# Optimization experiments

Hardware: AMD Instinct MI355X
Metric: run time of the kernel (lower is better)

## Reference

```python
import jax, jax.numpy as jnp
import numpy as np

B, L, E, H, NBF = 4, 4096, 512, 8, 256
D = E // H          # head_dim = 64
CHUNK = 256         # chunk size for exact causal linear attention
EPS = 1e-4          # stabilizer from performer softmax_kernel


def _orth_proj(nb, d, seed=0):
    """Gaussian orthogonal random features matrix [nb, d] (FAVOR+, scaling=0)."""
    rng = np.random.default_rng(seed)
    blocks = []
    n_full = nb // d
    for _ in range(n_full):
        q, _ = np.linalg.qr(rng.standard_normal((d, d)))
        blocks.append(q.T)
    rem = nb - n_full * d
    if rem:
        q, _ = np.linalg.qr(rng.standard_normal((d, d)))
        blocks.append(q.T[:rem])
    proj = np.concatenate(blocks, 0)
    mult = np.linalg.norm(rng.standard_normal((nb, d)), axis=1)  # chi(d) row scales
    return (mult[:, None] * proj).astype(np.float32)


def setup_inputs() -> dict:
    key = jax.random.key(0)
    ks = jax.random.split(key, 7)
    g = lambda k, sh: jax.random.normal(k, sh, dtype=jnp.float32)
    return {
        "queries": g(ks[0], (B, L, E)),
        "keys": g(ks[1], (B, L, E)),
        "values": g(ks[2], (B, L, E)),
        "Wq": g(ks[3], (D, D)) / np.float32(np.sqrt(D)),
        "Wk": g(ks[4], (D, D)) / np.float32(np.sqrt(D)),
        "Wv": g(ks[5], (D, D)) / np.float32(np.sqrt(D)),
        "Wout": g(ks[6], (E, E)) / np.float32(np.sqrt(E)),
        "bout": jnp.zeros((E,), jnp.float32),
        "proj": jnp.asarray(_orth_proj(NBF, D)),
    }


def _softmax_kernel(x, proj, is_query):
    # x: [B,H,L,D], proj: [M,D]  -> phi(x): [B,H,L,M]
    dn = x.shape[-1] ** -0.25
    ratio = proj.shape[0] ** -0.5
    xd = jnp.einsum('bhld,md->bhlm', x * dn, proj)
    diag = 0.5 * (dn ** 2) * jnp.sum(x * x, axis=-1, keepdims=True)
    if is_query:
        m = jnp.max(xd, axis=-1, keepdims=True)
    else:
        m = jnp.max(xd)
    return ratio * (jnp.exp(xd - diag - m) + EPS)


def _causal_linear_attn(qp, kp, v, chunk=CHUNK):
    # Exact causal linear attention via chunked prefix-state scan (no [B,H,L,M,D] tensor).
    Bn, Hn, Ln, M = qp.shape
    Dv = v.shape[-1]
    n = Ln // chunk
    qc = qp.reshape(Bn, Hn, n, chunk, M).transpose(2, 0, 1, 3, 4)
    kc = kp.reshape(Bn, Hn, n, chunk, M).transpose(2, 0, 1, 3, 4)
    vc = v.reshape(Bn, Hn, n, chunk, Dv).transpose(2, 0, 1, 3, 4)
    mask = jnp.tril(jnp.ones((chunk, chunk), qp.dtype))

    def step(carry, xs):
        S, z = carry                      # S:[B,H,M,D], z:[B,H,M]
        q, k, vv = xs                     # [B,H,C,M], [B,H,C,M], [B,H,C,D]
        scores = jnp.einsum('bhim,bhjm->bhij', q, k) * mask
        num = jnp.einsum('bhim,bhmd->bhid', q, S) + jnp.einsum('bhij,bhjd->bhid', scores, vv)
        den = jnp.einsum('bhim,bhm->bhi', q, z) + scores.sum(-1)
        out = num / den[..., None]
        S = S + jnp.einsum('bhjm,bhjd->bhmd', k, vv)
        z = z + k.sum(axis=2)
        return (S, z), out

    S0 = jnp.zeros((Bn, Hn, M, Dv), qp.dtype)
    z0 = jnp.zeros((Bn, Hn, M), qp.dtype)
    _, out = jax.lax.scan(step, (S0, z0), (qc, kc, vc))
    return out.transpose(1, 2, 0, 3, 4).reshape(Bn, Hn, Ln, Dv)


def reference(queries, keys, values, Wq, Wk, Wv, Wout, bout, proj):
    split = lambda x: x.reshape(B, L, H, D).transpose(0, 2, 1, 3)  # [B,H,L,D]
    q = split(queries) @ Wq.T
    k = split(keys) @ Wk.T
    v = split(values) @ Wv.T
    qp = _softmax_kernel(q, proj, True)
    kp = _softmax_kernel(k, proj, False)
    attn = _causal_linear_attn(qp, kp, v)
    attn = attn.transpose(0, 2, 1, 3).reshape(B, L, E)
    return attn @ Wout.T + bout
```

## Files before the change

### kernel.cpp

```cpp
#include <hip/hip_runtime.h>
#include <hip/hip_bf16.h>


#define BB 4
#define LL 4096
#define EE 512
#define HH 8
#define DD 64
#define MM 256
#define CC 128
#define NCH 32
#define BHN 32

constexpr float DN    = 0.35355339059327373f;
constexpr float DIAGC = 0.0625f;
constexpr float RATIO = 0.0625f;
constexpr float EPSV  = 1e-4f;
constexpr float L2E   = 1.4426950408889634f;
constexpr float CEPS  = 6.25e-6f;

typedef __attribute__((ext_vector_type(8))) short bf16x8;
typedef __attribute__((ext_vector_type(4))) float f32x4;
union FU { uint4 u; bf16x8 b; };
__device__ __forceinline__ bf16x8 asb(uint4 u){ FU f; f.u = u; return f.b; }
union PK8 { unsigned short s[8]; uint4 u; };
union PK4 { unsigned short s[4]; uint2 u; };

__device__ __forceinline__ unsigned short f2bf(float f){
  unsigned u = __float_as_uint(f);
  u = u + 0x7FFFu + ((u >> 16) & 1u);
  return (unsigned short)(u >> 16);
}
__device__ __forceinline__ float bfl(unsigned u){ return __uint_as_float(u << 16); }
__device__ __forceinline__ unsigned bfpair(float lo, float hi){
  return (unsigned)f2bf(lo) | ((unsigned)f2bf(hi) << 16);
}
__device__ __forceinline__ float pexp(float x, float nb){
  return exp2f(fmaf(x, L2E, nb)) + CEPS;
}
__device__ __forceinline__ unsigned enc_f32(float f){
  unsigned u = __float_as_uint(f);
  return (u & 0x80000000u) ? ~u : (u | 0x80000000u);
}
__device__ __forceinline__ float dec_f32(unsigned u){
  unsigned v = (u & 0x80000000u) ? (u & 0x7FFFFFFFu) : ~u;
  return __uint_as_float(v);
}
__device__ __forceinline__ uint4 pack8(float4 a, float4 b){
  PK8 p;
  p.s[0] = f2bf(a.x); p.s[1] = f2bf(a.y); p.s[2] = f2bf(a.z); p.s[3] = f2bf(a.w);
  p.s[4] = f2bf(b.x); p.s[5] = f2bf(b.y); p.s[6] = f2bf(b.z); p.s[7] = f2bf(b.w);
  return p.u;
}

__global__ __launch_bounds__(256) void k_cvt(const float* __restrict__ Wout,
                                             unsigned short* __restrict__ Woutb,
                                             const float* __restrict__ proj,
                                             unsigned short* __restrict__ projb){
  int bid = blockIdx.x, tid = threadIdx.x;
  if (bid < 512){
    int idx = bid * 256 + tid;
    float2 v = reinterpret_cast<const float2*>(Wout)[idx];
    reinterpret_cast<unsigned*>(Woutb)[idx] = bfpair(v.x, v.y);
  } else {
    int idx = (bid - 512) * 256 + tid;
    float2 v = reinterpret_cast<const float2*>(proj)[idx];
    reinterpret_cast<unsigned*>(projb)[idx] = bfpair(v.x * DN, v.y * DN);
  }
}

__global__ __launch_bounds__(256) void k_qkv(const float* __restrict__ xq,
                                             const float* __restrict__ xk,
                                             const float* __restrict__ xv,
                                             const float* __restrict__ Wq,
                                             const float* __restrict__ Wk,
                                             const float* __restrict__ Wv,
                                             unsigned short* __restrict__ qhb,
                                             unsigned short* __restrict__ khb,
                                             unsigned short* __restrict__ vTb,
                                             float* __restrict__ rsq,
                                             float* __restrict__ rsk){
  __shared__ unsigned short Wl[3 * 64 * 64];
  int tid = threadIdx.x;
  for (int idx = tid; idx < 3 * 64 * 8; idx += 256){
    int sel = idx >> 9, rem = idx & 511, row = rem >> 3, ch = rem & 7;
    const float* Wp = sel == 0 ? Wq : (sel == 1 ? Wk : Wv);
    const float4* w4 = reinterpret_cast<const float4*>(Wp) + row * 16 + ch * 2;
    int byte = sel * 8192 + row * 128 + ((ch * 16) ^ ((row & 7) << 4));
    *reinterpret_cast<uint4*>(reinterpret_cast<char*>(Wl) + byte) = pack8(w4[0], w4[1]);
  }
  __syncthreads();
  int w = tid >> 6, lane = tid & 63, l15 = lane & 15, g = lane >> 4;
  int bh = blockIdx.x >> 5, lb = blockIdx.x & 31;
  int b = bh >> 3, h = bh & 7;
  const char* Wc = reinterpret_cast<const char*>(Wl);
  #pragma unroll
  for (int tt = 0; tt < 2; ++tt){
    int lt = w * 2 + tt;
    int l = lb * 128 + lt * 16 + l15;
    size_t xoff = ((size_t)(b * LL + l)) * EE + h * DD;
    const float4* q4 = reinterpret_cast<const float4*>(xq + xoff);
    const float4* k4 = reinterpret_cast<const float4*>(xk + xoff);
    const float4* v4 = reinterpret_cast<const float4*>(xv + xoff);
    uint4 fq[2], fk[2], fv[2];
    #pragma unroll
    for (int ks = 0; ks < 2; ++ks){
      int fi = ks * 8 + g * 2;
      fq[ks] = pack8(q4[fi], q4[fi + 1]);
      fk[ks] = pack8(k4[fi], k4[fi + 1]);
      fv[ks] = pack8(v4[fi], v4[fi + 1]);
    }
    size_t grow = (size_t)bh * LL + l;
    {
      float ss = 0.f;
      #pragma unroll
      for (int dt = 0; dt < 4; ++dt){
        int row = dt * 16 + l15;
        f32x4 acc = {0.f, 0.f, 0.f, 0.f};
        #pragma unroll
        for (int ks = 0; ks < 2; ++ks){
          int byte = 0 * 8192 + row * 128 + ((ks * 64 + g * 16) ^ ((row & 7) << 4));
          uint4 wf = *reinterpret_cast<const uint4*>(Wc + byte);
          acc = __builtin_amdgcn_mfma_f32_16x16x32_bf16(asb(wf), asb(fq[ks]), acc, 0, 0, 0);
        }
        ss += acc[0]*acc[0] + acc[1]*acc[1] + acc[2]*acc[2] + acc[3]*acc[3];
        ushort4 pk;
        pk.x = f2bf(acc[0]); pk.y = f2bf(acc[1]); pk.z = f2bf(acc[2]); pk.w = f2bf(acc[3]);
        *reinterpret_cast<ushort4*>(qhb + grow * 64 + dt * 16 + g * 4) = pk;
      }
      ss += __shfl_xor(ss, 16, 64);
      ss += __shfl_xor(ss, 32, 64);
      if (g == 0) rsq[grow] = ss;
    }
    {
      float ss = 0.f;
      #pragma unroll
      for (int dt = 0; dt < 4; ++dt){
        int row = dt * 16 + l15;
        f32x4 acc = {0.f, 0.f, 0.f, 0.f};
        #pragma unroll
        for (int ks = 0; ks < 2; ++ks){
          int byte = 1 * 8192 + row * 128 + ((ks * 64 + g * 16) ^ ((row & 7) << 4));
          uint4 wf = *reinterpret_cast<const uint4*>(Wc + byte);
          acc = __builtin_amdgcn_mfma_f32_16x16x32_bf16(asb(wf), asb(fk[ks]), acc, 0, 0, 0);
        }
        ss += acc[0]*acc[0] + acc[1]*acc[1] + acc[2]*acc[2] + acc[3]*acc[3];
        ushort4 pk;
        pk.x = f2bf(acc[0]); pk.y = f2bf(acc[1]); pk.z = f2bf(acc[2]); pk.w = f2bf(acc[3]);
        *reinterpret_cast<ushort4*>(khb + grow * 64 + dt * 16 + g * 4) = pk;
      }
      ss += __shfl_xor(ss, 16, 64);
      ss += __shfl_xor(ss, 32, 64);
      if (g == 0) rsk[grow] = ss;
    }
    #pragma unroll
    for (int dt = 0; dt < 4; ++dt){
      int row = dt * 16 + l15;
      f32x4 acc = {0.f, 0.f, 0.f, 0.f};
      #pragma unroll
      for (int ks = 0; ks < 2; ++ks){
        int byte = 2 * 8192 + row * 128 + ((ks * 64 + g * 16) ^ ((row & 7) << 4));
        uint4 wf = *reinterpret_cast<const uint4*>(Wc + byte);
        acc = __builtin_amdgcn_mfma_f32_16x16x32_bf16(asb(fv[ks]), asb(wf), acc, 0, 0, 0);
      }
      ushort4 pk;
      pk.x = f2bf(acc[0]); pk.y = f2bf(acc[1]); pk.z = f2bf(acc[2]); pk.w = f2bf(acc[3]);
      *reinterpret_cast<ushort4*>(vTb + ((size_t)(bh * DD + dt * 16 + l15)) * LL
                                  + lb * 128 + lt * 16 + g * 4) = pk;
    }
  }
}

__global__ __launch_bounds__(256) void k_kmaxM(const unsigned short* __restrict__ khb,
                                               const unsigned short* __restrict__ projb,
                                               unsigned* __restrict__ kmaxp){
  __shared__ float red[4];
  int tid = threadIdx.x;
  int w = tid >> 6, lane = tid & 63, l15 = lane & 15, g = lane >> 4;
  const uint4* kh4 = reinterpret_cast<const uint4*>(khb);
  const uint4* pj4 = reinterpret_cast<const uint4*>(projb);
  uint4 pa0[16], pa1[16];
  #pragma unroll
  for (int mt = 0; mt < 16; ++mt){
    pa0[mt] = pj4[(size_t)(mt * 16 + l15) * 8 + g];
    pa1[mt] = pj4[(size_t)(mt * 16 + l15) * 8 + 4 + g];
  }
  float mx = -3.0e38f;
  #pragma unroll
  for (int it = 0; it < 8; ++it){
    int rb = blockIdx.x * 4 + w + it * 1024;
    size_t row = (size_t)rb * 16 + l15;
    uint4 kb0 = kh4[row * 8 + g];
    uint4 kb1 = kh4[row * 8 + 4 + g];
    #pragma unroll
    for (int mt = 0; mt < 16; ++mt){
      f32x4 acc = {0.f, 0.f, 0.f, 0.f};
      acc = __builtin_amdgcn_mfma_f32_16x16x32_bf16(asb(pa0[mt]), asb(kb0), acc, 0, 0, 0);
      acc = __builtin_amdgcn_mfma_f32_16x16x32_bf16(asb(pa1[mt]), asb(kb1), acc, 0, 0, 0);
      mx = fmaxf(mx, fmaxf(fmaxf(acc[0], acc[1]), fmaxf(acc[2], acc[3])));
    }
  }
  #pragma unroll
  for (int off = 32; off >= 1; off >>= 1)
    mx = fmaxf(mx, __shfl_xor(mx, off, 64));
  if (lane == 0) red[w] = mx;
  __syncthreads();
  if (tid == 0){
    float m = fmaxf(fmaxf(red[0], red[1]), fmaxf(red[2], red[3]));
    atomicMax(kmaxp, enc_f32(m));
  }
}

__global__ __launch_bounds__(256, 2) void k_chunkKV6(const unsigned short* __restrict__ khb,
                                                     const unsigned short* __restrict__ projb,
                                                     const float* __restrict__ rsk,
                                                     const unsigned* __restrict__ kmaxp,
                                                     const unsigned short* __restrict__ vTb,
                                                     unsigned short* __restrict__ SpT,
                                                     float* __restrict__ zf){
  __shared__ unsigned kL[4 * 128 * 33];
  int tid = threadIdx.x;
  int w = tid >> 6, lane = tid & 63, l15 = lane & 15, g = lane >> 4;
  int blk = blockIdx.x;
  int bh = blk >> 5, c = blk & 31;
  float km = dec_f32(*kmaxp);
  const uint4* kh4 = reinterpret_cast<const uint4*>(khb);
  const uint4* pj4 = reinterpret_cast<const uint4*>(projb);
  const uint4* vTu = reinterpret_cast<const uint4*>(vTb);
  unsigned* kLw = kL + w * 128 * 33;
  const unsigned short* kL16w = reinterpret_cast<const unsigned short*>(kLw);

  uint4 kf0[8], kf1[8];
  float nbk[8];
  #pragma unroll
  for (int jt = 0; jt < 8; ++jt){
    size_t jrow = (size_t)bh * LL + c * CC + jt * 16 + l15;
    kf0[jt] = kh4[jrow * 8 + g];
    kf1[jt] = kh4[jrow * 8 + 4 + g];
    nbk[jt] = -fmaf(fmaf(DIAGC, rsk[jrow], km), L2E, 4.0f);
  }
  #pragma unroll
  for (int mt = 0; mt < 4; ++mt){
    int mrow = w * 64 + mt * 16 + l15;
    uint4 a0 = pj4[(size_t)mrow * 8 + g];
    uint4 a1 = pj4[(size_t)mrow * 8 + 4 + g];
    #pragma unroll
    for (int jt = 0; jt < 8; ++jt){
      f32x4 acc = {0.f, 0.f, 0.f, 0.f};
      acc = __builtin_amdgcn_mfma_f32_16x16x32_bf16(asb(a0), asb(kf0[jt]), acc, 0, 0, 0);
      acc = __builtin_amdgcn_mfma_f32_16x16x32_bf16(asb(a1), asb(kf1[jt]), acc, 0, 0, 0);
      int dwi = (jt * 16 + l15) * 33 + mt * 8 + g * 2;
      kLw[dwi]     = bfpair(pexp(acc[0], nbk[jt]), pexp(acc[1], nbk[jt]));
      kLw[dwi + 1] = bfpair(pexp(acc[2], nbk[jt]), pexp(acc[3], nbk[jt]));
    }
  }

  uint4 vf[4][4];
  #pragma unroll
  for (int dt = 0; dt < 4; ++dt)
    #pragma unroll
    for (int ks = 0; ks < 4; ++ks)
      vf[dt][ks] = vTu[((size_t)(bh * DD + dt * 16 + l15)) * 512 + c * 16 + ks * 4 + g];

  uint4 zero4 = {0u, 0u, 0u, 0u};
  uint4 ones4 = {0x3F803F80u, 0x3F803F80u, 0x3F803F80u, 0x3F803F80u};
  uint4 onesf = (l15 == 0) ? ones4 : zero4;

  #pragma unroll
  for (int mtr = 0; mtr < 4; ++mtr){
    f32x4 acc[4];
    #pragma unroll
    for (int dt = 0; dt < 4; ++dt) acc[dt] = (f32x4){0.f, 0.f, 0.f, 0.f};
    f32x4 accz = {0.f, 0.f, 0.f, 0.f};
    #pragma unroll
    for (int ks = 0; ks < 4; ++ks){
      PK8 p;
      #pragma unroll
      for (int e = 0; e < 8; ++e)
        p.s[e] = kL16w[(ks * 32 + g * 8 + e) * 66 + mtr * 16 + l15];
      bf16x8 kfb = asb(p.u);
      #pragma unroll
      for (int dt = 0; dt < 4; ++dt)
        acc[dt] = __builtin_amdgcn_mfma_f32_16x16x32_bf16(kfb, asb(vf[dt][ks]), acc[dt], 0, 0, 0);
      accz = __builtin_amdgcn_mfma_f32_16x16x32_bf16(kfb, asb(onesf), accz, 0, 0, 0);
    }
    int m0 = w * 64 + mtr * 16;
    #pragma unroll
    for (int dt = 0; dt < 4; ++dt){
      ushort4 pk;
      pk.x = f2bf(acc[dt][0]); pk.y = f2bf(acc[dt][1]);
      pk.z = f2bf(acc[dt][2]); pk.w = f2bf(acc[dt][3]);
      *reinterpret_cast<ushort4*>(SpT + ((size_t)blk * DD + dt * 16 + l15) * MM + m0 + g * 4) = pk;
    }
    if (l15 == 0){
      float4 o; o.x = accz[0]; o.y = accz[1]; o.z = accz[2]; o.w = accz[3];
      *reinterpret_cast<float4*>(zf + (size_t)blk * MM + m0 + g * 4) = o;
    }
  }
}

__global__ __launch_bounds__(256) void k_prefix(unsigned short* __restrict__ buf,
                                                const float* __restrict__ zf,
                                                unsigned short* __restrict__ zb){
  int bid = blockIdx.x, tid = threadIdx.x;
  if (bid < 512){
    const int per4 = (DD * MM) / 4;
    int idx = bid * 256 + tid;
    int bh = idx / per4, r4 = idx - bh * per4;
    float run[4];
    #pragma unroll
    for (int e = 0; e < 4; ++e) run[e] = 0.f;
    for (int c = 0; c < NCH; ++c){
      size_t a = (((size_t)bh * NCH + c) * (DD * MM)) >> 2;
      uint2* p = reinterpret_cast<uint2*>(buf) + a + r4;
      uint2 v = *p;
      PK4 t; t.u = v;
      PK4 o;
      #pragma unroll
      for (int e = 0; e < 4; ++e){
        o.s[e] = f2bf(run[e]);
        run[e] += bfl((unsigned)t.s[e]);
      }
      *p = o.u;
    }
  } else {
    const int per8 = MM / 8;
    int idx = (bid - 512) * 256 + tid;
    int bh = idx / per8, r8 = idx - bh * per8;
    float run[8];
    #pragma unroll
    for (int e = 0; e < 8; ++e) run[e] = 0.f;
    for (int c = 0; c < NCH; ++c){
      size_t base = ((size_t)bh * NCH + c) * MM + r8 * 8;
      float4 v0 = *reinterpret_cast<const float4*>(zf + base);
      float4 v1 = *reinterpret_cast<const float4*>(zf + base + 4);
      PK8 o;
      #pragma unroll
      for (int e = 0; e < 8; ++e) o.s[e] = f2bf(run[e]);
      run[0] += v0.x; run[1] += v0.y; run[2] += v0.z; run[3] += v0.w;
      run[4] += v1.x; run[5] += v1.y; run[6] += v1.z; run[7] += v1.w;
      *reinterpret_cast<uint4*>(zb + base) = o.u;
    }
  }
}

__global__ __launch_bounds__(256, 2) void k_cattn12(const unsigned short* __restrict__ qhb,
                                                    const unsigned short* __restrict__ khb,
                                                    const unsigned short* __restrict__ projb,
                                                    const float* __restrict__ rsq,
                                                    const float* __restrict__ rsk,
                                                    const unsigned* __restrict__ kmaxp,
                                                    const unsigned short* __restrict__ vTb,
                                                    const unsigned short* __restrict__ Spb,
                                                    const unsigned short* __restrict__ zb,
                                                    unsigned short* __restrict__ attnb){
  __shared__ unsigned LDSU[20480];
  char* lds = reinterpret_cast<char*>(LDSU);
  int tid = threadIdx.x;
  int w = tid >> 6, lane = tid & 63, l15 = lane & 15, g = lane >> 4;
  int blk = blockIdx.x;
  int bh = blk >> 5, c = blk & 31;
  int b = bh >> 3, h = bh & 7;
  size_t grow0 = (size_t)bh * LL + c * CC;
  float km = dec_f32(*kmaxp);
  const uint4* qh4 = reinterpret_cast<const uint4*>(qhb);
  const uint4* kh4 = reinterpret_cast<const uint4*>(khb);
  const uint4* pj4 = reinterpret_cast<const uint4*>(projb);
  const uint4* vTu = reinterpret_cast<const uint4*>(vTb);
  const uint4* Spu = reinterpret_cast<const uint4*>(Spb);
  const uint4* zbu = reinterpret_cast<const uint4*>(zb);
  uint4 zero4 = {0u, 0u, 0u, 0u};
  uint4 ones4 = {0x3F803F80u, 0x3F803F80u, 0x3F803F80u, 0x3F803F80u};
  int swz = (l15 & 7) << 4;

  {
    uint4 kf0[8], kf1[8];
    float nbk[8];
    #pragma unroll
    for (int jt = 0; jt < 8; ++jt){
      size_t jrow = grow0 + jt * 16 + l15;
      kf0[jt] = kh4[jrow * 8 + g];
      kf1[jt] = kh4[jrow * 8 + 4 + g];
      nbk[jt] = -fmaf(fmaf(DIAGC, rsk[jrow], km), L2E, 4.0f);
    }
    #pragma unroll
    for (int mt = 0; mt < 4; ++mt){
      int mrow = w * 64 + mt * 16 + l15;
      uint4 a0 = pj4[(size_t)mrow * 8 + g];
      uint4 a1 = pj4[(size_t)mrow * 8 + 4 + g];
      #pragma unroll
      for (int jt = 0; jt < 8; ++jt){
        int jr = jt * 16 + l15;
        f32x4 acc = {0.f, 0.f, 0.f, 0.f};
        acc = __builtin_amdgcn_mfma_f32_16x16x32_bf16(asb(a0), asb(kf0[jt]), acc, 0, 0, 0);
        acc = __builtin_amdgcn_mfma_f32_16x16x32_bf16(asb(a1), asb(kf1[jt]), acc, 0, 0, 0);
        uint2 u;
        u.x = bfpair(pexp(acc[0], nbk[jt]), pexp(acc[1], nbk[jt]));
        u.y = bfpair(pexp(acc[2], nbk[jt]), pexp(acc[3], nbk[jt]));
        int byte = jr * 512 + ((w * 128 + mt * 32 + g * 8) ^ ((jr & 7) << 4));
        *reinterpret_cast<uint2*>(lds + byte) = u;
      }
    }
  }

  int its[2] = { w, 7 - w };
  int swb = 65536 + w * 4096 + l15 * 256;
  uint4 qf[2][8];
  f32x4 acc[2][5];
  {
    size_t irow0 = grow0 + its[0] * 16 + l15;
    size_t irow1 = grow0 + its[1] * 16 + l15;
    uint4 qb0_0 = qh4[irow0 * 8 + g];
    uint4 qb1_0 = qh4[irow0 * 8 + 4 + g];
    uint4 qb0_1 = qh4[irow1 * 8 + g];
    uint4 qb1_1 = qh4[irow1 * 8 + 4 + g];
    f32x4 aq0[16], aq1[16];
    #pragma unroll
    for (int mt = 0; mt < 16; ++mt){
      uint4 a0 = pj4[(size_t)(mt * 16 + l15) * 8 + g];
      uint4 a1 = pj4[(size_t)(mt * 16 + l15) * 8 + 4 + g];
      f32x4 x0 = {0.f, 0.f, 0.f, 0.f};
      x0 = __builtin_amdgcn_mfma_f32_16x16x32_bf16(asb(a0), asb(qb0_0), x0, 0, 0, 0);
      aq0[mt] = __builtin_amdgcn_mfma_f32_16x16x32_bf16(asb(a1), asb(qb1_0), x0, 0, 0, 0);
      f32x4 x1 = {0.f, 0.f, 0.f, 0.f};
      x1 = __builtin_amdgcn_mfma_f32_16x16x32_bf16(asb(a0), asb(qb0_1), x1, 0, 0, 0);
      aq1[mt] = __builtin_amdgcn_mfma_f32_16x16x32_bf16(asb(a1), asb(qb1_1), x1, 0, 0, 0);
    }
    {
      float mx = -3.0e38f;
      #pragma unroll
      for (int mt = 0; mt < 16; ++mt)
        mx = fmaxf(mx, fmaxf(fmaxf(aq0[mt][0], aq0[mt][1]), fmaxf(aq0[mt][2], aq0[mt][3])));
      mx = fmaxf(mx, __shfl_xor(mx, 16, 64));
      mx = fmaxf(mx, __shfl_xor(mx, 32, 64));
      float nb = -fmaf(fmaf(DIAGC, rsq[irow0], mx), L2E, 4.0f);
      #pragma unroll
      for (int half = 0; half < 2; ++half){
        #pragma unroll
        for (int mt = 0; mt < 8; ++mt){
          f32x4 a = aq0[half * 8 + mt];
          uint2 u;
          u.x = bfpair(pexp(a[0], nb), pexp(a[1], nb));
          u.y = bfpair(pexp(a[2], nb), pexp(a[3], nb));
          int byte = swb + ((mt * 32 + g * 8) ^ swz);
          *reinterpret_cast<uint2*>(lds + byte) = u;
        }
        #pragma unroll
        for (int ks = 0; ks < 4; ++ks){
          int byte = swb + ((ks * 64 + g * 16) ^ swz);
          qf[0][half * 4 + ks] = *reinterpret_cast<const uint4*>(lds + byte);
        }
      }
    }
    {
      float mx = -3.0e38f;
      #pragma unroll
      for (int mt = 0; mt < 16; ++mt)
        mx = fmaxf(mx, fmaxf(fmaxf(aq1[mt][0], aq1[mt][1]), fmaxf(aq1[mt][2], aq1[mt][3])));
      mx = fmaxf(mx, __shfl_xor(mx, 16, 64));
      mx = fmaxf(mx, __shfl_xor(mx, 32, 64));
      float nb = -fmaf(fmaf(DIAGC, rsq[irow1], mx), L2E, 4.0f);
      #pragma unroll
      for (int half = 0; half < 2; ++half){
        #pragma unroll
        for (int mt = 0; mt < 8; ++mt){
          f32x4 a = aq1[half * 8 + mt];
          uint2 u;
          u.x = bfpair(pexp(a[0], nb), pexp(a[1], nb));
          u.y = bfpair(pexp(a[2], nb), pexp(a[3], nb));
          int byte = swb + ((mt * 32 + g * 8) ^ swz);
          *reinterpret_cast<uint2*>(lds + byte) = u;
        }
        #pragma unroll
        for (int ks = 0; ks < 4; ++ks){
          int byte = swb + ((ks * 64 + g * 16) ^ swz);
          qf[1][half * 4 + ks] = *reinterpret_cast<const uint4*>(lds + byte);
        }
      }
    }
  }

  #pragma unroll
  for (int t = 0; t < 2; ++t)
    #pragma unroll
    for (int a5 = 0; a5 < 5; ++a5) acc[t][a5] = (f32x4){0.f, 0.f, 0.f, 0.f};
  #pragma unroll
  for (int ks = 0; ks < 8; ++ks){
    bf16x8 q0 = asb(qf[0][ks]);
    bf16x8 q1 = asb(qf[1][ks]);
    #pragma unroll
    for (int dt = 0; dt < 4; ++dt){
      uint4 spf = Spu[((size_t)blk * DD + dt * 16 + l15) * 32 + ks * 4 + g];
      acc[0][dt] = __builtin_amdgcn_mfma_f32_16x16x32_bf16(asb(spf), q0, acc[0][dt], 0, 0, 0);
      acc[1][dt] = __builtin_amdgcn_mfma_f32_16x16x32_bf16(asb(spf), q1, acc[1][dt], 0, 0, 0);
    }
    uint4 zfr = (l15 == 0) ? zbu[blk * 32 + ks * 4 + g] : zero4;
    acc[0][4] = __builtin_amdgcn_mfma_f32_16x16x32_bf16(asb(zfr), q0, acc[0][4], 0, 0, 0);
    acc[1][4] = __builtin_amdgcn_mfma_f32_16x16x32_bf16(asb(zfr), q1, acc[1][4], 0, 0, 0);
  }

  uint4 vf[4][4];
  #pragma unroll
  for (int dt = 0; dt < 4; ++dt)
    #pragma unroll
    for (int ks = 0; ks < 4; ++ks)
      vf[dt][ks] = vTu[((size_t)(bh * DD + dt * 16 + l15)) * 512 + c * 16 + ks * 4 + g];
  __syncthreads();

  #pragma unroll
  for (int t = 0; t < 2; ++t){
    int it = its[t];
    int i = it * 16 + l15;
    int jtmax = it | 1;
    #pragma unroll
    for (int jt = 0; jt < 8; ++jt){
      if (jt <= jtmax){
        f32x4 sa0 = {0.f, 0.f, 0.f, 0.f};
        f32x4 sa1 = {0.f, 0.f, 0.f, 0.f};
        int jr = jt * 16 + l15;
        __builtin_amdgcn_s_setprio(1);
        #pragma unroll
        for (int ks = 0; ks < 4; ++ks){
          int byte0 = jr * 512 + (((2 * ks) * 64 + g * 16) ^ ((jr & 7) << 4));
          int byte1 = jr * 512 + (((2 * ks + 1) * 64 + g * 16) ^ ((jr & 7) << 4));
          uint4 kfu0 = *reinterpret_cast<const uint4*>(lds + byte0);
          uint4 kfu1 = *reinterpret_cast<const uint4*>(lds + byte1);
          sa0 = __builtin_amdgcn_mfma_f32_16x16x32_bf16(asb(kfu0), asb(qf[t][2 * ks]), sa0, 0, 0, 0);
          sa1 = __builtin_amdgcn_mfma_f32_16x16x32_bf16(asb(kfu1), asb(qf[t][2 * ks + 1]), sa1, 0, 0, 0);
        }
        __builtin_amdgcn_s_setprio(0);
        f32x4 sa = sa0 + sa1;
        int jb = jt * 16 + g * 4;
        uint2 u;
        u.x = bfpair((jb + 0 <= i) ? sa[0] : 0.f, (jb + 1 <= i) ? sa[1] : 0.f);
        u.y = bfpair((jb + 2 <= i) ? sa[2] : 0.f, (jb + 3 <= i) ? sa[3] : 0.f);
        int byte = swb + ((jt * 32 + g * 8) ^ swz);
        *reinterpret_cast<uint2*>(lds + byte) = u;
      }
    }
    int ksmax = it >> 1;
    #pragma unroll
    for (int ks = 0; ks < 4; ++ks){
      if (ks <= ksmax){
        int byte = swb + ((ks * 64 + g * 16) ^ swz);
        uint4 sfu = *reinterpret_cast<const uint4*>(lds + byte);
        bf16x8 sf = asb(sfu);
        __builtin_amdgcn_s_setprio(1);
        #pragma unroll
        for (int dt = 0; dt < 4; ++dt)
          acc[t][dt] = __builtin_amdgcn_mfma_f32_16x16x32_bf16(asb(vf[dt][ks]), sf, acc[t][dt], 0, 0, 0);
        uint4 of = (l15 == 0) ? ones4 : zero4;
        acc[t][4] = __builtin_amdgcn_mfma_f32_16x16x32_bf16(asb(of), sf, acc[t][4], 0, 0, 0);
        __builtin_amdgcn_s_setprio(0);
      }
    }
    float den = __shfl(acc[t][4][0], l15, 64);
    float inv = 1.f / den;
    size_t obase = ((size_t)(b * LL + c * CC + i)) * EE + h * DD;
    #pragma unroll
    for (int dt = 0; dt < 4; ++dt){
      ushort4 pk;
      pk.x = f2bf(acc[t][dt][0] * inv); pk.y = f2bf(acc[t][dt][1] * inv);
      pk.z = f2bf(acc[t][dt][2] * inv); pk.w = f2bf(acc[t][dt][3] * inv);
      *reinterpret_cast<ushort4*>(attnb + obase + dt * 16 + g * 4) = pk;
    }
  }
}

__global__ __launch_bounds__(256, 2) void k_proj_M2(const unsigned short* __restrict__ attnb,
                                                    const unsigned short* __restrict__ Woutb,
                                                    const float* __restrict__ bout,
                                                    float* __restrict__ out){
  __shared__ unsigned short Wl[64 * 512];
  int tid = threadIdx.x;
  int w = tid >> 6, lane = tid & 63, l15 = lane & 15, g = lane >> 4;
  int rb = blockIdx.x & 63, eb = blockIdx.x >> 6;
  int r0 = rb * 256, e0 = eb * 64;
  const uint4* at4 = reinterpret_cast<const uint4*>(attnb);
  const uint4* Wo4 = reinterpret_cast<const uint4*>(Woutb);
  for (int idx = tid; idx < 4096; idx += 256){
    int row = idx >> 6, rest = idx & 63, kt = rest >> 3, ch = rest & 7;
    uint4 v = Wo4[(size_t)(e0 + row) * 64 + kt * 8 + ch];
    int byte = kt * 8192 + row * 128 + ((ch * 16) ^ ((row & 7) << 4));
    *reinterpret_cast<uint4*>(reinterpret_cast<char*>(Wl) + byte) = v;
  }
  __syncthreads();
  const char* Wc = reinterpret_cast<const char*>(Wl);
  f32x4 acc[4][4];
  #pragma unroll
  for (int rt = 0; rt < 4; ++rt)
    #pragma unroll
    for (int ct = 0; ct < 4; ++ct) acc[rt][ct] = (f32x4){0.f, 0.f, 0.f, 0.f};
  size_t rbase = (size_t)(r0 + w * 64 + l15) * 64;
  #pragma unroll 4
  for (int ks = 0; ks < 16; ++ks){
    uint4 bfr[4];
    #pragma unroll
    for (int rt = 0; rt < 4; ++rt)
      bfr[rt] = at4[rbase + (size_t)rt * 16 * 64 + ks * 4 + g];
    int kt = ks >> 1, k2 = ks & 1;
    #pragma unroll
    for (int ct = 0; ct < 4; ++ct){
      int row = ct * 16 + l15;
      int byte = kt * 8192 + row * 128 + ((k2 * 64 + g * 16) ^ ((row & 7) << 4));
      uint4 af = *reinterpret_cast<const uint4*>(Wc + byte);
      bf16x8 afb = asb(af);
      #pragma unroll
      for (int rt = 0; rt < 4; ++rt)
        acc[rt][ct] = __builtin_amdgcn_mfma_f32_16x16x32_bf16(afb, asb(bfr[rt]), acc[rt][ct], 0, 0, 0);
    }
  }
  #pragma unroll
  for (int ct = 0; ct < 4; ++ct){
    int e = e0 + ct * 16 + g * 4;
    float4 bo = *reinterpret_cast<const float4*>(bout + e);
    #pragma unroll
    for (int rt = 0; rt < 4; ++rt){
      int r = r0 + w * 64 + rt * 16 + l15;
      float4 o;
      o.x = acc[rt][ct][0] + bo.x; o.y = acc[rt][ct][1] + bo.y;
      o.z = acc[rt][ct][2] + bo.z; o.w = acc[rt][ct][3] + bo.w;
      *reinterpret_cast<float4*>(out + (size_t)r * EE + e) = o;
    }
  }
}

extern "C" void kernel_launch(void* const* d_in, const int* in_sizes, int n_in,
                              void* d_out, int out_size, void* d_ws, size_t ws_size,
                              hipStream_t stream){
  const float* queries = (const float*)d_in[0];
  const float* keys    = (const float*)d_in[1];
  const float* values  = (const float*)d_in[2];
  const float* Wq      = (const float*)d_in[3];
  const float* Wk      = (const float*)d_in[4];
  const float* Wv      = (const float*)d_in[5];
  const float* Wout    = (const float*)d_in[6];
  const float* bout    = (const float*)d_in[7];
  const float* proj    = (const float*)d_in[8];

  char* ws = (char*)d_ws;
  unsigned short* qhb  = (unsigned short*)(ws + 0);
  unsigned short* khb  = (unsigned short*)(ws + 16777216);
  unsigned short* vTb  = (unsigned short*)(ws + 33554432);
  unsigned short* SpT  = (unsigned short*)(ws + 50331648);
  unsigned short* attnb= (unsigned short*)(ws + 83886080);
  float*          zfbuf= (float*)(ws + 100663296);
  unsigned short* zb   = (unsigned short*)(ws + 101711872);
  float*          rsq  = (float*)(ws + 102236160);
  float*          rsk  = (float*)(ws + 102760448);
  unsigned short* Woutb= (unsigned short*)(ws + 103284736);
  unsigned short* projb= (unsigned short*)(ws + 103809024);
  unsigned*       kmax = (unsigned*)(ws + 103841792);
  float*          out  = (float*)d_out;

  hipMemsetAsync(kmax, 0, 4, stream);

  k_cvt<<<dim3(544), dim3(256), 0, stream>>>(Wout, Woutb, proj, projb);

  k_qkv<<<dim3(BHN * 32), dim3(256), 0, stream>>>(queries, keys, values, Wq, Wk, Wv,
                                                  qhb, khb, vTb, rsq, rsk);

  k_kmaxM<<<dim3(256), dim3(256), 0, stream>>>(khb, projb, kmax);

  k_chunkKV6<<<dim3(BHN * NCH), dim3(256), 0, stream>>>(khb, projb, rsk, kmax, vTb, SpT, zfbuf);

  k_prefix<<<dim3(516), dim3(256), 0, stream>>>(SpT, zfbuf, zb);

  k_cattn12<<<dim3(BHN * NCH), dim3(256), 0, stream>>>(qhb, khb, projb, rsq, rsk, kmax,
                                                       vTb, SpT, zb, attnb);

  k_proj_M2<<<dim3(512), dim3(256), 0, stream>>>(attnb, Woutb, bout, out);
}
```

Measured before the change: 190.7 us.

## Fold key max reduction into QKV kernel using premultiplied proj·Wk matrix

Precomputes a bf16 matrix equal to proj times Wk, scaled by DN, in the conversion kernel. The QKV kernel then computes key feature logits straight from the raw key fragments and reduces the global max with an atomic. This removes the separate k_kmaxM launch and its re-read of khb. The max is now taken from logits built with a differently rounded product, so it may differ slightly from the logits used later. The prefix-scan loops also get unroll pragmas.

Measured after the change: 205.8 us. 7.9% more time.

```diff
diff --git a/kernel.cpp b/kernel.cpp
--- a/kernel.cpp
+++ b/kernel.cpp
@@ -56,16 +56,26 @@
 __global__ __launch_bounds__(256) void k_cvt(const float* __restrict__ Wout,
                                              unsigned short* __restrict__ Woutb,
                                              const float* __restrict__ proj,
-                                             unsigned short* __restrict__ projb){
+                                             unsigned short* __restrict__ projb,
+                                             const float* __restrict__ Wk,
+                                             unsigned short* __restrict__ PWb){
   int bid = blockIdx.x, tid = threadIdx.x;
   if (bid < 512){
     int idx = bid * 256 + tid;
     float2 v = reinterpret_cast<const float2*>(Wout)[idx];
     reinterpret_cast<unsigned*>(Woutb)[idx] = bfpair(v.x, v.y);
-  } else {
+  } else if (bid < 544){
     int idx = (bid - 512) * 256 + tid;
     float2 v = reinterpret_cast<const float2*>(proj)[idx];
     reinterpret_cast<unsigned*>(projb)[idx] = bfpair(v.x * DN, v.y * DN);
+  } else {
+    int idx = (bid - 544) * 256 + tid;
+    int m = idx >> 6, dp = idx & 63;
+    float s = 0.f;
+    #pragma unroll 8
+    for (int d = 0; d < 64; ++d)
+      s += proj[m * 64 + d] * Wk[d * 64 + dp];
+    PWb[idx] = f2bf(DN * s);
   }
 }
 
@@ -75,12 +85,15 @@
                                              const float* __restrict__ Wq,
                                              const float* __restrict__ Wk,
                                              const float* __restrict__ Wv,
+                                             const unsigned short* __restrict__ PWb,
                                              unsigned short* __restrict__ qhb,
                                              unsigned short* __restrict__ khb,
                                              unsigned short* __restrict__ vTb,
                                              float* __restrict__ rsq,
-                                             float* __restrict__ rsk){
+                                             float* __restrict__ rsk,
+                                             unsigned* __restrict__ kmaxp){
   __shared__ unsigned short Wl[3 * 64 * 64];
+  __shared__ float red[4];
   int tid = threadIdx.x;
   for (int idx = tid; idx < 3 * 64 * 8; idx += 256){
     int sel = idx >> 9, rem = idx & 511, row = rem >> 3, ch = rem & 7;
@@ -94,6 +107,8 @@
   int bh = blockIdx.x >> 5, lb = blockIdx.x & 31;
   int b = bh >> 3, h = bh & 7;
   const char* Wc = reinterpret_cast<const char*>(Wl);
+  const uint4* pw4 = reinterpret_cast<const uint4*>(PWb);
+  float mxk = -3.0e38f;
   #pragma unroll
   for (int tt = 0; tt < 2; ++tt){
     int lt = w * 2 + tt;
@@ -154,6 +169,15 @@
       if (g == 0) rsk[grow] = ss;
     }
     #pragma unroll
+    for (int mt = 0; mt < 16; ++mt){
+      uint4 a0 = pw4[(size_t)(mt * 16 + l15) * 8 + g];
+      uint4 a1 = pw4[(size_t)(mt * 16 + l15) * 8 + 4 + g];
+      f32x4 acc = {0.f, 0.f, 0.f, 0.f};
+      acc = __builtin_amdgcn_mfma_f32_16x16x32_bf16(asb(a0), asb(fk[0]), acc, 0, 0, 0);
+      acc = __builtin_amdgcn_mfma_f32_16x16x32_bf16(asb(a1), asb(fk[1]), acc, 0, 0, 0);
+      mxk = fmaxf(mxk, fmaxf(fmaxf(acc[0], acc[1]), fmaxf(acc[2], acc[3])));
+    }
+    #pragma unroll
     for (int dt = 0; dt < 4; ++dt){
       int row = dt * 16 + l15;
       f32x4 acc = {0.f, 0.f, 0.f, 0.f};
@@ -169,41 +193,10 @@
                                   + lb * 128 + lt * 16 + g * 4) = pk;
     }
   }
-}
-
-__global__ __launch_bounds__(256) void k_kmaxM(const unsigned short* __restrict__ khb,
-                                               const unsigned short* __restrict__ projb,
-                                               unsigned* __restrict__ kmaxp){
-  __shared__ float red[4];
-  int tid = threadIdx.x;
-  int w = tid >> 6, lane = tid & 63, l15 = lane & 15, g = lane >> 4;
-  const uint4* kh4 = reinterpret_cast<const uint4*>(khb);
-  const uint4* pj4 = reinterpret_cast<const uint4*>(projb);
-  uint4 pa0[16], pa1[16];
-  #pragma unroll
-  for (int mt = 0; mt < 16; ++mt){
-    pa0[mt] = pj4[(size_t)(mt * 16 + l15) * 8 + g];
-    pa1[mt] = pj4[(size_t)(mt * 16 + l15) * 8 + 4 + g];
-  }
-  float mx = -3.0e38f;
-  #pragma unroll
-  for (int it = 0; it < 8; ++it){
-    int rb = blockIdx.x * 4 + w + it * 1024;
-    size_t row = (size_t)rb * 16 + l15;
-    uint4 kb0 = kh4[row * 8 + g];
-    uint4 kb1 = kh4[row * 8 + 4 + g];
-    #pragma unroll
-    for (int mt = 0; mt < 16; ++mt){
-      f32x4 acc = {0.f, 0.f, 0.f, 0.f};
-      acc = __builtin_amdgcn_mfma_f32_16x16x32_bf16(asb(pa0[mt]), asb(kb0), acc, 0, 0, 0);
-      acc = __builtin_amdgcn_mfma_f32_16x16x32_bf16(asb(pa1[mt]), asb(kb1), acc, 0, 0, 0);
-      mx = fmaxf(mx, fmaxf(fmaxf(acc[0], acc[1]), fmaxf(acc[2], acc[3])));
-    }
-  }
   #pragma unroll
   for (int off = 32; off >= 1; off >>= 1)
-    mx = fmaxf(mx, __shfl_xor(mx, off, 64));
-  if (lane == 0) red[w] = mx;
+    mxk = fmaxf(mxk, __shfl_xor(mxk, off, 64));
+  if (lane == 0) red[w] = mxk;
   __syncthreads();
   if (tid == 0){
     float m = fmaxf(fmaxf(red[0], red[1]), fmaxf(red[2], red[3]));
@@ -310,6 +303,7 @@
     float run[4];
     #pragma unroll
     for (int e = 0; e < 4; ++e) run[e] = 0.f;
+    #pragma unroll 4
     for (int c = 0; c < NCH; ++c){
       size_t a = (((size_t)bh * NCH + c) * (DD * MM)) >> 2;
       uint2* p = reinterpret_cast<uint2*>(buf) + a + r4;
@@ -330,6 +324,7 @@
     float run[8];
     #pragma unroll
     for (int e = 0; e < 8; ++e) run[e] = 0.f;
+    #pragma unroll 4
     for (int c = 0; c < NCH; ++c){
       size_t base = ((size_t)bh * NCH + c) * MM + r8 * 8;
       float4 v0 = *reinterpret_cast<const float4*>(zf + base);
@@ -650,17 +645,16 @@
   float*          rsk  = (float*)(ws + 102760448);
   unsigned short* Woutb= (unsigned short*)(ws + 103284736);
   unsigned short* projb= (unsigned short*)(ws + 103809024);
-  unsigned*       kmax = (unsigned*)(ws + 103841792);
+  unsigned short* PWb  = (unsigned short*)(ws + 103841792);
+  unsigned*       kmax = (unsigned*)(ws + 103874560);
   float*          out  = (float*)d_out;
 
   hipMemsetAsync(kmax, 0, 4, stream);
 
-  k_cvt<<<dim3(544), dim3(256), 0, stream>>>(Wout, Woutb, proj, projb);
-
-  k_qkv<<<dim3(BHN * 32), dim3(256), 0, stream>>>(queries, keys, values, Wq, Wk, Wv,
-                                                  qhb, khb, vTb, rsq, rsk);
-
-  k_kmaxM<<<dim3(256), dim3(256), 0, stream>>>(khb, projb, kmax);
+  k_cvt<<<dim3(608), dim3(256), 0, stream>>>(Wout, Woutb, proj, projb, Wk, PWb);
+
+  k_qkv<<<dim3(BHN * 32), dim3(256), 0, stream>>>(queries, keys, values, Wq, Wk, Wv, PWb,
+                                                  qhb, khb, vTb, rsq, rsk, kmax);
 
   k_chunkKV6<<<dim3(BHN * NCH), dim3(256), 0, stream>>>(khb, projb, rsk, kmax, vTb, SpT, zfbuf);
 
```
